# Performance work log

Measured on AMD Instinct MI355X. Metric: run time of the kernel, lower is better.

Reference implementation:

```python
import jax, jax.numpy as jnp
import numpy as np

VOCAB = 150
EOS = 2
PAD = 0
EPS = 1e-8


def _ngram_penalty_sum(tokens, n):
    # tokens: [B, S] int. Returns sum over batch of (count-2)*0.1*n for each
    # ngram repeated >=3 times. Equivalent trick: hash each ngram to a unique
    # int (base-VOCAB encoding), sort per row; a position is a 3rd-or-later
    # occurrence iff sorted[i] == sorted[i-2]; the number of such positions
    # equals sum over unique ngrams of max(count-2, 0).
    B, S = tokens.shape
    if S < n * 3:
        return jnp.float32(0.0)
    L = S - n + 1
    h = sum(tokens[:, j:j + L].astype(jnp.int32) * (VOCAB ** j) for j in range(n))
    hs = jnp.sort(h, axis=1)
    rep = jnp.sum(hs[:, 2:] == hs[:, :-2], axis=1)  # [B]
    return jnp.sum(rep.astype(jnp.float32)) * (0.1 * n)


def setup_inputs() -> dict:
    key = jax.random.key(0)
    k1, k2, k3 = jax.random.split(key, 3)
    B, S, V, IN = 256, 512, VOCAB, 512
    predictions = jax.random.normal(k1, (B, S, V), dtype=jnp.float32)
    targets = jax.random.randint(k2, (B, S), 0, V)
    attention_weights = jax.random.uniform(k3, (B, S, IN), dtype=jnp.float32)
    return {"predictions": predictions, "targets": targets,
            "attention_weights": attention_weights}


def reference(predictions, targets, attention_weights):
    B, S, V = predictions.shape

    # --- main NLL loss (ignore_index=PAD, mean over non-pad) ---
    mask = (targets != PAD).astype(predictions.dtype)  # [B,S]
    gathered = jnp.take_along_axis(predictions, targets[..., None], axis=-1)[..., 0]
    main = -jnp.sum(gathered * mask) / jnp.maximum(jnp.sum(mask), 1.0)

    # --- pattern penalty on argmax tokens ---
    pred_tokens = jnp.argmax(predictions, axis=-1)  # [B,S]
    pattern = (_ngram_penalty_sum(pred_tokens, 2)
               + _ngram_penalty_sum(pred_tokens, 3)
               + _ngram_penalty_sum(pred_tokens, 4)) / B

    # --- EOS encouragement ---
    eos_mask = (targets == EOS).astype(predictions.dtype)  # [B,S]
    eos_probs = jax.nn.softmax(predictions, axis=-1)[:, :, EOS]  # [B,S]
    eos_loss = -jnp.mean(eos_mask * jnp.log(eos_probs + EPS))
    eos_loss = jnp.where(jnp.sum(eos_mask) > 0, eos_loss, 0.0)
    has_eos_t = jnp.any(targets == EOS, axis=1)
    has_eos_p = jnp.any(pred_tokens == EOS, axis=1)
    no_eos = jnp.mean((has_eos_t & ~has_eos_p).astype(predictions.dtype))
    eos_total = eos_loss + 0.5 * no_eos

    # --- attention diversity (negative mean entropy, scaled) ---
    ent = -jnp.sum(attention_weights * jnp.log(attention_weights + EPS), axis=-1)
    attention = -jnp.mean(ent) * 0.1

    total = main + 0.1 * pattern + 0.2 * eos_total + 0.05 * attention
    return jnp.stack([total, main, pattern, eos_total, attention])
```

## Files before the change

### kernel.cpp

```cpp
#include <hip/hip_runtime.h>
#include <math.h>

#define BB   256
#define SS   512
#define VV   150
#define INW  512
#define NPOS (BB * SS)
#define GRID 2048
#define EPSF 1e-8f

typedef float vf4 __attribute__((ext_vector_type(4)));


__global__ __launch_bounds__(256) void kern_ab(
    const float* __restrict__ pred, const int* __restrict__ tgt,
    const float* __restrict__ attw, float4* __restrict__ pA,
    float* __restrict__ pB, unsigned char* __restrict__ toks,
    int* __restrict__ counter)
{
    __shared__ float shp[16];
    __shared__ float shb[4];
    const int tid  = threadIdx.x;
    const int lane = tid & 63;
    const int wid  = tid >> 6;

    if (blockIdx.x == 0 && tid == 0) *counter = 0;

    const int gw = blockIdx.x * 4 + wid;
    float s_g = 0.f, s_mc = 0.f, s_el = 0.f, s_ec = 0.f;
    for (int it = 0; it < 16; ++it) {
        const int pos = gw + it * 8192;
        const float* row = pred + (size_t)pos * VV;
        const float v0 = row[lane];
        const float v1 = row[lane + 64];
        const bool  l3 = lane < (VV - 128);
        const float v2 = l3 ? row[lane + 128] : -INFINITY;

        float m = fmaxf(fmaxf(v0, v1), v2);
        #pragma unroll
        for (int off = 32; off > 0; off >>= 1)
            m = fmaxf(m, __shfl_xor(m, off));
        int li = (v0 == m) ? lane : (v1 == m) ? lane + 64
                 : (l3 && v2 == m) ? lane + 128 : (1 << 20);
        #pragma unroll
        for (int off = 32; off > 0; off >>= 1)
            li = min(li, __shfl_xor(li, off));

        const int t = tgt[pos];
        const float src = (t < 64) ? v0 : (t < 128) ? v1 : v2;
        const float g = __shfl(src, t & 63);

        if (t == 2) {
            float ex = __expf(v0 - m) + __expf(v1 - m)
                     + (l3 ? __expf(v2 - m) : 0.f);
            #pragma unroll
            for (int off = 32; off > 0; off >>= 1)
                ex += __shfl_xor(ex, off);
            const float p2 = __shfl(v0, 2);
            if (lane == 0) {
                s_el += __logf(__expf(p2 - m) / ex + EPSF);
                s_ec += 1.f;
            }
        }
        if (lane == 0) {
            toks[pos] = (unsigned char)li;
            if (t != 0) { s_g += g; s_mc += 1.f; }
        }
    }
    if (lane == 0) {
        shp[wid * 4 + 0] = s_g;  shp[wid * 4 + 1] = s_mc;
        shp[wid * 4 + 2] = s_el; shp[wid * 4 + 3] = s_ec;
    }

    const vf4* a4 = (const vf4*)attw;
    const size_t base = (size_t)blockIdx.x * 8192;
    float s = 0.f;
    #pragma unroll 8
    for (int it = 0; it < 32; ++it) {
        const vf4 v = __builtin_nontemporal_load(a4 + base + it * 256 + tid);
        s += v.x * __logf(v.x + EPSF) + v.y * __logf(v.y + EPSF)
           + v.z * __logf(v.z + EPSF) + v.w * __logf(v.w + EPSF);
    }
    #pragma unroll
    for (int off = 32; off > 0; off >>= 1) s += __shfl_xor(s, off);
    if (lane == 0) shb[wid] = s;

    __syncthreads();
    if (tid == 0) {
        float4 r;
        r.x = shp[0] + shp[4] + shp[8]  + shp[12];
        r.y = shp[1] + shp[5] + shp[9]  + shp[13];
        r.z = shp[2] + shp[6] + shp[10] + shp[14];
        r.w = shp[3] + shp[7] + shp[11] + shp[15];
        pA[blockIdx.x] = r;
        pB[blockIdx.x] = shb[0] + shb[1] + shb[2] + shb[3];
    }
}

__global__ __launch_bounds__(256) void kern_cf(
    const unsigned char* __restrict__ toks, const int* __restrict__ tgt,
    int* __restrict__ pC, int* __restrict__ hasx, int* __restrict__ counter,
    const float4* __restrict__ pA, const float* __restrict__ pB,
    float* __restrict__ out)
{
    const int blk = blockIdx.x;
    const int b = blk & 255;
    const int n = 2 + (blk >> 8);
    const int L = SS - n + 1;
    const int tid = threadIdx.x;

    __shared__ int tok[SS];
    __shared__ __align__(16) int h[SS];
    __shared__ int sflags;
    __shared__ int sticket;

    if (tid == 0) sflags = 0;
    const unsigned char* rt = toks + b * SS;
    tok[tid]       = rt[tid];
    tok[tid + 256] = rt[tid + 256];
    __syncthreads();

    if (blk < 256) {
        const int* trow = tgt + b * SS;
        int f = 0;
        if (trow[tid] == 2 || trow[tid + 256] == 2) f |= 1;
        if (tok[tid] == 2 || tok[tid + 256] == 2)   f |= 2;
        if (f) atomicOr(&sflags, f);
    }

    #pragma unroll
    for (int q = 0; q < 2; ++q) {
        const int i = tid + q * 256;
        int hv;
        if (i < L) {
            hv = tok[i];
            int mul = VV;
            for (int j = 1; j < n; ++j) { hv += tok[i + j] * mul; mul *= VV; }
        } else {
            hv = 0x7F000000 + i;
        }
        h[i] = hv;
    }
    __syncthreads();

    const int i1 = tid, i2 = tid + 256;
    const int h1 = h[i1], h2 = h[i2];
    int c1 = 0, c2 = 0;
    #pragma unroll 4
    for (int j = 0; j < SS; j += 4) {
        const int4 hv = *(const int4*)&h[j];
        c1 += (hv.x == h1 && j     < i1) + (hv.y == h1 && j + 1 < i1)
            + (hv.z == h1 && j + 2 < i1) + (hv.w == h1 && j + 3 < i1);
        c2 += (hv.x == h2 && j     < i2) + (hv.y == h2 && j + 1 < i2)
            + (hv.z == h2 && j + 2 < i2) + (hv.w == h2 && j + 3 < i2);
    }
    int rep = (c1 >= 2) + (c2 >= 2);
    #pragma unroll
    for (int off = 32; off > 0; off >>= 1) rep += __shfl_xor(rep, off);
    __shared__ int w4[4];
    if ((tid & 63) == 0) w4[tid >> 6] = rep;
    __syncthreads();
    if (tid == 0) {
        pC[blk] = w4[0] + w4[1] + w4[2] + w4[3];
        if (blk < 256) hasx[b] = ((sflags & 1) && !(sflags & 2)) ? 1 : 0;
        __threadfence();
        sticket = atomicAdd(counter, 1);
    }
    __syncthreads();
    if (sticket != 768 - 1) return;

    __threadfence();
    const int lane = tid & 63;
    const int wid  = tid >> 6;
    double v[9];
    #pragma unroll
    for (int k = 0; k < 9; ++k) v[k] = 0.0;
    for (int i = tid; i < GRID; i += 256) {
        const float4 p = pA[i];
        v[0] += p.x; v[1] += p.y; v[2] += p.z; v[3] += p.w;
    }
    for (int i = tid; i < GRID; i += 256) v[4] += pB[i];
    v[5] = pC[tid]; v[6] = pC[tid + 256]; v[7] = pC[tid + 512];
    v[8] = (double)hasx[tid];

    #pragma unroll
    for (int off = 32; off > 0; off >>= 1)
        #pragma unroll
        for (int k = 0; k < 9; ++k) v[k] += __shfl_xor(v[k], off);

    __shared__ double sd[4][9];
    if (lane == 0)
        for (int k = 0; k < 9; ++k) sd[wid][k] = v[k];
    __syncthreads();

    if (tid == 0) {
        double r[9];
        for (int k = 0; k < 9; ++k) r[k] = sd[0][k] + sd[1][k] + sd[2][k] + sd[3][k];
        const double mainv    = -r[0] / fmax(r[1], 1.0);
        const double eos_loss = (r[3] > 0.0) ? (-r[2] / (double)NPOS) : 0.0;
        const double no_eos   = r[8] / (double)BB;
        const double eos_tot  = eos_loss + 0.5 * no_eos;
        const double att      = 0.1 * r[4] / (double)NPOS;
        const double pattern  = (0.2 * r[5] + 0.3 * r[6] + 0.4 * r[7]) / (double)BB;
        const double total    = mainv + 0.1 * pattern + 0.2 * eos_tot + 0.05 * att;
        out[0] = (float)total;   out[1] = (float)mainv; out[2] = (float)pattern;
        out[3] = (float)eos_tot; out[4] = (float)att;
    }
}

extern "C" void kernel_launch(void* const* d_in, const int* in_sizes, int n_in,
                              void* d_out, int out_size, void* d_ws, size_t ws_size,
                              hipStream_t stream)
{
    const float* pred = (const float*)d_in[0];
    const int*   tgt  = (const int*)d_in[1];
    const float* attw = (const float*)d_in[2];
    float* out = (float*)d_out;
    char*  ws  = (char*)d_ws;

    float4* pA   = (float4*)ws;
    float*  pB   = (float*)(ws + 32768);
    int*    pC   = (int*)(ws + 40960);
    int*    hasx = (int*)(ws + 44032);
    int*    cnt  = (int*)(ws + 45056);
    unsigned char* toks = (unsigned char*)(ws + 45312);

    kern_ab<<<GRID, 256, 0, stream>>>(pred, tgt, attw, pA, pB, toks, cnt);
    kern_cf<<<768, 256, 0, stream>>>(toks, tgt, pC, hasx, cnt, pA, pB, out);
}
```

Baseline: 100.6 us.

## Use atomic work-stealing task queue and packed-key argmax in fused reduction kernel

Replaces the static per-block split with a persistent loop in which each block takes tasks from a global atomic counter. Tasks are either 32 prediction rows or 4096 float4 chunks of the attention weights, which is meant to balance load between the two memory streams. Argmax is now a single 64-bit packed-key max reduction instead of separate max and index reductions, and eight tokens are written per store. The change adds a memset launch and a separate counter for the second kernel, and drops the nontemporal loads on the attention weights.

```diff
diff --git a/kernel.cpp b/kernel.cpp
--- a/kernel.cpp
+++ b/kernel.cpp
@@ -4,96 +4,124 @@
 #define BB   256
 #define SS   512
 #define VV   150
-#define INW  512
 #define NPOS (BB * SS)
 #define GRID 2048
+#define A_TASKS 4096
+#define B_TASKS 4096
+#define N_TASKS (A_TASKS + B_TASKS)
 #define EPSF 1e-8f
 
-typedef float vf4 __attribute__((ext_vector_type(4)));
-
+
+__device__ __forceinline__ unsigned long long akey(float f, int idx) {
+    unsigned u = __float_as_uint(f);
+    unsigned mono = ((int)u >= 0) ? (u | 0x80000000u) : ~u;
+    return ((unsigned long long)mono << 8) | (unsigned)(255 - idx);
+}
+__device__ __forceinline__ unsigned long long kmax(unsigned long long a,
+                                                   unsigned long long b) {
+    return a > b ? a : b;
+}
 
 __global__ __launch_bounds__(256) void kern_ab(
     const float* __restrict__ pred, const int* __restrict__ tgt,
     const float* __restrict__ attw, float4* __restrict__ pA,
     float* __restrict__ pB, unsigned char* __restrict__ toks,
-    int* __restrict__ counter)
+    int* __restrict__ cnt)
 {
-    __shared__ float shp[16];
-    __shared__ float shb[4];
+    __shared__ int stask;
     const int tid  = threadIdx.x;
     const int lane = tid & 63;
-    const int wid  = tid >> 6;
-
-    if (blockIdx.x == 0 && tid == 0) *counter = 0;
-
-    const int gw = blockIdx.x * 4 + wid;
-    float s_g = 0.f, s_mc = 0.f, s_el = 0.f, s_ec = 0.f;
-    for (int it = 0; it < 16; ++it) {
-        const int pos = gw + it * 8192;
-        const float* row = pred + (size_t)pos * VV;
-        const float v0 = row[lane];
-        const float v1 = row[lane + 64];
-        const bool  l3 = lane < (VV - 128);
-        const float v2 = l3 ? row[lane + 128] : -INFINITY;
-
-        float m = fmaxf(fmaxf(v0, v1), v2);
-        #pragma unroll
-        for (int off = 32; off > 0; off >>= 1)
-            m = fmaxf(m, __shfl_xor(m, off));
-        int li = (v0 == m) ? lane : (v1 == m) ? lane + 64
-                 : (l3 && v2 == m) ? lane + 128 : (1 << 20);
-        #pragma unroll
-        for (int off = 32; off > 0; off >>= 1)
-            li = min(li, __shfl_xor(li, off));
-
-        const int t = tgt[pos];
-        const float src = (t < 64) ? v0 : (t < 128) ? v1 : v2;
-        const float g = __shfl(src, t & 63);
-
-        if (t == 2) {
-            float ex = __expf(v0 - m) + __expf(v1 - m)
-                     + (l3 ? __expf(v2 - m) : 0.f);
+    const int w    = tid >> 6;
+
+    for (;;) {
+        __syncthreads();
+        if (tid == 0) stask = atomicAdd(cnt, 1);
+        __syncthreads();
+        const int task = stask;
+        if (task >= N_TASKS) break;
+
+        if (task < A_TASKS) {
+            const int pbase = task * 32 + w * 8;
+            float sg = 0.f, smc = 0.f, sel = 0.f, sec = 0.f;
+            unsigned long long tok8 = 0;
+            for (int p = 0; p < 8; ++p) {
+                const int pos = pbase + p;
+                const float* row = pred + (size_t)pos * VV;
+                const float v0 = row[lane];
+                const float v1 = row[lane + 64];
+                const bool  l3 = lane < (VV - 128);
+                const float v2 = l3 ? row[lane + 128] : 0.f;
+
+                unsigned long long k = kmax(akey(v0, lane), akey(v1, lane + 64));
+                if (l3) k = kmax(k, akey(v2, lane + 128));
+                #pragma unroll
+                for (int off = 32; off > 0; off >>= 1)
+                    k = kmax(k, __shfl_xor(k, off));
+                const int li = 255 - (int)(k & 0xFF);
+
+                const int t = tgt[pos];
+                const float src = (t < 64) ? v0 : (t < 128) ? v1 : v2;
+                const float g = __shfl(src, t & 63);
+
+                if (t == 2) {
+                    const unsigned mono = (unsigned)(k >> 8);
+                    const unsigned fb = (mono & 0x80000000u) ? (mono & 0x7FFFFFFFu)
+                                                             : ~mono;
+                    const float m = __uint_as_float(fb);
+                    float ex = __expf(v0 - m) + __expf(v1 - m)
+                             + (l3 ? __expf(v2 - m) : 0.f);
+                    #pragma unroll
+                    for (int off = 32; off > 0; off >>= 1)
+                        ex += __shfl_xor(ex, off);
+                    const float p2 = __shfl(v0, 2);
+                    if (lane == 0) {
+                        sel += __logf(__expf(p2 - m) / ex + EPSF);
+                        sec += 1.f;
+                    }
+                }
+                if (lane == 0) {
+                    tok8 |= (unsigned long long)li << (8 * p);
+                    if (t != 0) { sg += g; smc += 1.f; }
+                }
+            }
+            if (lane == 0) {
+                *(unsigned long long*)(toks + pbase) = tok8;
+            }
+            __shared__ float red[4][4];
+            if (lane == 0) {
+                red[w][0] = sg; red[w][1] = smc; red[w][2] = sel; red[w][3] = sec;
+            }
+            __syncthreads();
+            if (tid == 0) {
+                float4 r;
+                r.x = red[0][0] + red[1][0] + red[2][0] + red[3][0];
+                r.y = red[0][1] + red[1][1] + red[2][1] + red[3][1];
+                r.z = red[0][2] + red[1][2] + red[2][2] + red[3][2];
+                r.w = red[0][3] + red[1][3] + red[2][3] + red[3][3];
+                pA[task] = r;
+            }
+        } else {
+            const int j = task - A_TASKS;
+            const float4* a4 = (const float4*)attw;
+            const size_t base = (size_t)j * 4096;
+            float s0 = 0.f, s1 = 0.f;
             #pragma unroll
-            for (int off = 32; off > 0; off >>= 1)
-                ex += __shfl_xor(ex, off);
-            const float p2 = __shfl(v0, 2);
-            if (lane == 0) {
-                s_el += __logf(__expf(p2 - m) / ex + EPSF);
-                s_ec += 1.f;
-            }
+            for (int k = 0; k < 16; k += 2) {
+                const float4 x = a4[base + (size_t)k * 256 + tid];
+                const float4 y = a4[base + (size_t)(k + 1) * 256 + tid];
+                s0 += x.x * __logf(x.x + EPSF) + x.y * __logf(x.y + EPSF)
+                    + x.z * __logf(x.z + EPSF) + x.w * __logf(x.w + EPSF);
+                s1 += y.x * __logf(y.x + EPSF) + y.y * __logf(y.y + EPSF)
+                    + y.z * __logf(y.z + EPSF) + y.w * __logf(y.w + EPSF);
+            }
+            float s = s0 + s1;
+            #pragma unroll
+            for (int off = 32; off > 0; off >>= 1) s += __shfl_xor(s, off);
+            __shared__ float redb[4];
+            if (lane == 0) redb[w] = s;
+            __syncthreads();
+            if (tid == 0) pB[j] = redb[0] + redb[1] + redb[2] + redb[3];
         }
-        if (lane == 0) {
-            toks[pos] = (unsigned char)li;
-            if (t != 0) { s_g += g; s_mc += 1.f; }
-        }
-    }
-    if (lane == 0) {
-        shp[wid * 4 + 0] = s_g;  shp[wid * 4 + 1] = s_mc;
-        shp[wid * 4 + 2] = s_el; shp[wid * 4 + 3] = s_ec;
-    }
-
-    const vf4* a4 = (const vf4*)attw;
-    const size_t base = (size_t)blockIdx.x * 8192;
-    float s = 0.f;
-    #pragma unroll 8
-    for (int it = 0; it < 32; ++it) {
-        const vf4 v = __builtin_nontemporal_load(a4 + base + it * 256 + tid);
-        s += v.x * __logf(v.x + EPSF) + v.y * __logf(v.y + EPSF)
-           + v.z * __logf(v.z + EPSF) + v.w * __logf(v.w + EPSF);
-    }
-    #pragma unroll
-    for (int off = 32; off > 0; off >>= 1) s += __shfl_xor(s, off);
-    if (lane == 0) shb[wid] = s;
-
-    __syncthreads();
-    if (tid == 0) {
-        float4 r;
-        r.x = shp[0] + shp[4] + shp[8]  + shp[12];
-        r.y = shp[1] + shp[5] + shp[9]  + shp[13];
-        r.z = shp[2] + shp[6] + shp[10] + shp[14];
-        r.w = shp[3] + shp[7] + shp[11] + shp[15];
-        pA[blockIdx.x] = r;
-        pB[blockIdx.x] = shb[0] + shb[1] + shb[2] + shb[3];
     }
 }
 
@@ -175,11 +203,11 @@
     double v[9];
     #pragma unroll
     for (int k = 0; k < 9; ++k) v[k] = 0.0;
-    for (int i = tid; i < GRID; i += 256) {
+    for (int i = tid; i < A_TASKS; i += 256) {
         const float4 p = pA[i];
         v[0] += p.x; v[1] += p.y; v[2] += p.z; v[3] += p.w;
     }
-    for (int i = tid; i < GRID; i += 256) v[4] += pB[i];
+    for (int i = tid; i < B_TASKS; i += 256) v[4] += pB[i];
     v[5] = pC[tid]; v[6] = pC[tid + 256]; v[7] = pC[tid + 512];
     v[8] = (double)hasx[tid];
 
@@ -219,12 +247,13 @@
     char*  ws  = (char*)d_ws;
 
     float4* pA   = (float4*)ws;
-    float*  pB   = (float*)(ws + 32768);
-    int*    pC   = (int*)(ws + 40960);
-    int*    hasx = (int*)(ws + 44032);
-    int*    cnt  = (int*)(ws + 45056);
-    unsigned char* toks = (unsigned char*)(ws + 45312);
-
+    float*  pB   = (float*)(ws + 65536);
+    int*    pC   = (int*)(ws + 81920);
+    int*    hasx = (int*)(ws + 84992);
+    int*    cnt  = (int*)(ws + 86016);
+    unsigned char* toks = (unsigned char*)(ws + 86272);
+
+    hipMemsetAsync(cnt, 0, 8, stream);
     kern_ab<<<GRID, 256, 0, stream>>>(pred, tgt, attw, pA, pB, toks, cnt);
-    kern_cf<<<768, 256, 0, stream>>>(toks, tgt, pC, hasx, cnt, pA, pB, out);
-}
+    kern_cf<<<768, 256, 0, stream>>>(toks, tgt, pC, hasx, cnt + 1, pA, pB, out);
+}
```

Result: slower. 183.8 us (+82.7%).

## Interleave attention entropy loads with argmax loop, pack argmax key, trim ngram scans

Applied to the files above, without the earlier changes.

Attention-weight loads and entropy math move into the prediction-row loop, so both memory streams are in flight together instead of running as two separate phases, and the nontemporal load hint is dropped. The argmax now uses a single max-reduction over a packed 32-bit key (an order-preserving float with the low byte replaced by the inverted index) rather than separate max and index reductions. The max used for the EOS softmax is rebuilt from that key with its low 8 mantissa bits cleared, which shifts the subtracted max slightly but cancels in the ratio. Packing the index into the low byte means values that differ only in those bits compare as ties and resolve to the lower index, which may change argmax versus an exact comparison. The n-gram duplicate count loops stop at each element's own index instead of scanning the full row, though the two rows now run as separate loops of different lengths, which splits one wavefront's lanes across different trip counts.

```diff
diff --git a/kernel.cpp b/kernel.cpp
--- a/kernel.cpp
+++ b/kernel.cpp
@@ -4,13 +4,16 @@
 #define BB   256
 #define SS   512
 #define VV   150
-#define INW  512
 #define NPOS (BB * SS)
 #define GRID 2048
 #define EPSF 1e-8f
 
-typedef float vf4 __attribute__((ext_vector_type(4)));
-
+
+__device__ __forceinline__ unsigned key32(float f, int idx) {
+    const unsigned u = __float_as_uint(f);
+    const unsigned mono = ((int)u >= 0) ? (u | 0x80000000u) : ~u;
+    return (mono & 0xFFFFFF00u) | (unsigned)(255 - idx);
+}
 
 __global__ __launch_bounds__(256) void kern_ab(
     const float* __restrict__ pred, const int* __restrict__ tgt,
@@ -27,8 +30,16 @@
     if (blockIdx.x == 0 && tid == 0) *counter = 0;
 
     const int gw = blockIdx.x * 4 + wid;
+    const float4* a4 = (const float4*)attw;
+    const size_t bbase = (size_t)blockIdx.x * 8192;
+
     float s_g = 0.f, s_mc = 0.f, s_el = 0.f, s_ec = 0.f;
+    float s0 = 0.f, s1 = 0.f;
+
     for (int it = 0; it < 16; ++it) {
+        const float4 x0 = a4[bbase + (size_t)(2 * it)     * 256 + tid];
+        const float4 x1 = a4[bbase + (size_t)(2 * it + 1) * 256 + tid];
+
         const int pos = gw + it * 8192;
         const float* row = pred + (size_t)pos * VV;
         const float v0 = row[lane];
@@ -36,21 +47,23 @@
         const bool  l3 = lane < (VV - 128);
         const float v2 = l3 ? row[lane + 128] : -INFINITY;
 
-        float m = fmaxf(fmaxf(v0, v1), v2);
+        unsigned k = key32(v0, lane);
+        k = max(k, key32(v1, lane + 64));
+        if (l3) k = max(k, key32(v2, lane + 128));
         #pragma unroll
         for (int off = 32; off > 0; off >>= 1)
-            m = fmaxf(m, __shfl_xor(m, off));
-        int li = (v0 == m) ? lane : (v1 == m) ? lane + 64
-                 : (l3 && v2 == m) ? lane + 128 : (1 << 20);
-        #pragma unroll
-        for (int off = 32; off > 0; off >>= 1)
-            li = min(li, __shfl_xor(li, off));
+            k = max(k, __shfl_xor(k, off));
+        const int li = 255 - (int)(k & 0xFFu);
 
         const int t = tgt[pos];
         const float src = (t < 64) ? v0 : (t < 128) ? v1 : v2;
         const float g = __shfl(src, t & 63);
 
         if (t == 2) {
+            const unsigned mono_hi = k & 0xFFFFFF00u;
+            const float m = (mono_hi & 0x80000000u)
+                          ? __uint_as_float(mono_hi & 0x7FFFFFFFu)
+                          : __uint_as_float(~mono_hi);
             float ex = __expf(v0 - m) + __expf(v1 - m)
                      + (l3 ? __expf(v2 - m) : 0.f);
             #pragma unroll
@@ -66,21 +79,18 @@
             toks[pos] = (unsigned char)li;
             if (t != 0) { s_g += g; s_mc += 1.f; }
         }
-    }
+
+        s0 += x0.x * __logf(x0.x + EPSF) + x0.y * __logf(x0.y + EPSF)
+            + x0.z * __logf(x0.z + EPSF) + x0.w * __logf(x0.w + EPSF);
+        s1 += x1.x * __logf(x1.x + EPSF) + x1.y * __logf(x1.y + EPSF)
+            + x1.z * __logf(x1.z + EPSF) + x1.w * __logf(x1.w + EPSF);
+    }
+
     if (lane == 0) {
         shp[wid * 4 + 0] = s_g;  shp[wid * 4 + 1] = s_mc;
         shp[wid * 4 + 2] = s_el; shp[wid * 4 + 3] = s_ec;
     }
-
-    const vf4* a4 = (const vf4*)attw;
-    const size_t base = (size_t)blockIdx.x * 8192;
-    float s = 0.f;
-    #pragma unroll 8
-    for (int it = 0; it < 32; ++it) {
-        const vf4 v = __builtin_nontemporal_load(a4 + base + it * 256 + tid);
-        s += v.x * __logf(v.x + EPSF) + v.y * __logf(v.y + EPSF)
-           + v.z * __logf(v.z + EPSF) + v.w * __logf(v.w + EPSF);
-    }
+    float s = s0 + s1;
     #pragma unroll
     for (int off = 32; off > 0; off >>= 1) s += __shfl_xor(s, off);
     if (lane == 0) shb[wid] = s;
@@ -145,12 +155,16 @@
 
     const int i1 = tid, i2 = tid + 256;
     const int h1 = h[i1], h2 = h[i2];
+    const int bound1 = (i1 & ~3) + 4;
+    const int bound2 = (i2 & ~3) + 4;
     int c1 = 0, c2 = 0;
-    #pragma unroll 4
-    for (int j = 0; j < SS; j += 4) {
+    for (int j = 0; j < bound1; j += 4) {
         const int4 hv = *(const int4*)&h[j];
         c1 += (hv.x == h1 && j     < i1) + (hv.y == h1 && j + 1 < i1)
             + (hv.z == h1 && j + 2 < i1) + (hv.w == h1 && j + 3 < i1);
+    }
+    for (int j = 0; j < bound2; j += 4) {
+        const int4 hv = *(const int4*)&h[j];
         c2 += (hv.x == h2 && j     < i2) + (hv.y == h2 && j + 1 < i2)
             + (hv.z == h2 && j + 2 < i2) + (hv.w == h2 && j + 3 < i2);
     }
```

Measured after the change: 102.1 us. About the same (+1.5%).
